# Kernel tuning notes

Measured on AMD Instinct MI355X. Metric: run time of the kernel, lower is better.

Reference implementation:

```python
import jax, jax.numpy as jnp
import numpy as np

EPS = 1e-6
N = 512
D = 8192


def solve_lap_np(cost):
    """Jonker-Volgenant shortest-augmenting-path LAP (same optimum as
    scipy.optimize.linear_sum_assignment). Returns col4row: col assigned to each row."""
    cost = np.asarray(cost, dtype=np.float64)
    n = cost.shape[0]
    u = np.zeros(n)
    v = np.zeros(n)
    path = np.full(n, -1, dtype=np.int64)
    col4row = np.full(n, -1, dtype=np.int64)
    row4col = np.full(n, -1, dtype=np.int64)
    for cur_row in range(n):
        shortest = np.full(n, np.inf)
        SR = np.zeros(n, dtype=bool)  # visited rows
        SC = np.zeros(n, dtype=bool)  # visited cols
        i = cur_row
        min_val = 0.0
        sink = -1
        while sink == -1:
            SR[i] = True
            idx = np.nonzero(~SC)[0]
            r = min_val + cost[i, idx] - u[i] - v[idx]
            upd = r < shortest[idx]
            shortest[idx[upd]] = r[upd]
            path[idx[upd]] = i
            j = idx[np.argmin(shortest[idx])]
            min_val = shortest[j]
            SC[j] = True
            if row4col[j] == -1:
                sink = j
            else:
                i = row4col[j]
        # dual updates
        u[cur_row] += min_val
        sr = np.nonzero(SR)[0]
        sr = sr[sr != cur_row]
        u[sr] += min_val - shortest[col4row[sr]]
        sc = np.nonzero(SC)[0]
        v[sc] -= min_val - shortest[sc]
        # augment along the alternating path
        j = sink
        while True:
            i = path[j]
            row4col[j] = i
            col4row[i], j = j, col4row[i]
            if i == cur_row:
                break
    return col4row


def lap_assign(cost):
    """Optimal assignment as a one-hot labelling matrix (rows -> cols)."""
    n = cost.shape[0]
    col = jax.pure_callback(
        lambda c: solve_lap_np(np.asarray(c)).astype(np.int32),
        jax.ShapeDtypeStruct((n,), jnp.int32),
        cost,
    )
    return jax.nn.one_hot(col, n, dtype=cost.dtype)


def l2_normalize(x):
    # torch F.normalize(p=2, dim=1): x / max(||x||, eps)
    norm = jnp.sqrt(jnp.sum(x * x, axis=1, keepdims=True))
    return x / jnp.maximum(norm, EPS)


def setup_inputs() -> dict:
    key = jax.random.key(0)
    k1, k2, k3 = jax.random.split(key, 3)
    return {
        "un1": jax.random.normal(k1, (N, D), dtype=jnp.float32),
        "un2": jax.random.normal(k2, (N, D), dtype=jnp.float32),
        "un3": jax.random.normal(k3, (N, D), dtype=jnp.float32),
    }


def reference(un1, un2, un3):
    n1 = l2_normalize(un1)
    n2 = l2_normalize(un2)
    n3 = l2_normalize(un3)
    # cosine-distance cost matrices, cycle 1->2->3->1
    c12 = 1.0 - n1 @ n2.T
    c23 = 1.0 - n2 @ n3.T
    c31 = 1.0 - n3 @ n1.T
    x12 = lap_assign(c12)
    x23 = lap_assign(c23)
    x31 = lap_assign(c31)
    return (x12, x23, x31)
```

## Files before the change

kernel.cpp:

```cpp
#include <hip/hip_runtime.h>
#include <math.h>

#define NN 512
#define DD 8192

__global__ __launch_bounds__(256) void norm_kernel(
    const float* __restrict__ a0, const float* __restrict__ a1,
    const float* __restrict__ a2, float* __restrict__ scales) {
  const float* mats[3] = {a0, a1, a2};
  const int m = blockIdx.y;
  const int row = blockIdx.x;
  const float* x = mats[m] + (size_t)row * DD;
  const int tid = threadIdx.x;
  float s = 0.f;
  for (int k = tid * 4; k < DD; k += 256 * 4) {
    const float4 v = *(const float4*)(x + k);
    s += v.x * v.x + v.y * v.y + v.z * v.z + v.w * v.w;
  }
#pragma unroll
  for (int off = 32; off > 0; off >>= 1) s += __shfl_down(s, off);
  __shared__ float ws[4];
  if ((tid & 63) == 0) ws[tid >> 6] = s;
  __syncthreads();
  if (tid == 0) {
    const float t = ws[0] + ws[1] + ws[2] + ws[3];
    scales[m * NN + row] = 1.0f / fmaxf(sqrtf(t), 1e-6f);
  }
}

__global__ __launch_bounds__(512) void cost_gemm_kernel(
    const float* __restrict__ a0, const float* __restrict__ a1,
    const float* __restrict__ a2, const float* __restrict__ scales,
    float* __restrict__ cost_all) {
  const float* mats[3] = {a0, a1, a2};
  const int p = blockIdx.z;
  const int pA = p, pB = (p + 1) % 3;
  const float* A = mats[pA];
  const float* B = mats[pB];
  float* C = cost_all + (size_t)p * NN * NN;

  __shared__ float lds_a[32 * 64];
  __shared__ float lds_b[32 * 64];

  const int tid = threadIdx.x;
  const int rowBase = blockIdx.y * 64;
  const int colBase = blockIdx.x * 64;

  const int sr = tid & 63;
  const int sk = (tid >> 6) * 4;

  const float* Arow = A + (size_t)(rowBase + sr) * DD + sk;
  const float* Brow = B + (size_t)(colBase + sr) * DD + sk;

  const int tx = tid & 31;
  const int ty = tid >> 5;

  float acc[4][2];
#pragma unroll
  for (int i = 0; i < 4; ++i) {
    acc[i][0] = 0.f;
    acc[i][1] = 0.f;
  }

  for (int kb = 0; kb < DD; kb += 32) {
    const float4 av = *(const float4*)(Arow + kb);
    const float4 bv = *(const float4*)(Brow + kb);
    lds_a[(sk + 0) * 64 + sr] = av.x;
    lds_a[(sk + 1) * 64 + sr] = av.y;
    lds_a[(sk + 2) * 64 + sr] = av.z;
    lds_a[(sk + 3) * 64 + sr] = av.w;
    lds_b[(sk + 0) * 64 + sr] = bv.x;
    lds_b[(sk + 1) * 64 + sr] = bv.y;
    lds_b[(sk + 2) * 64 + sr] = bv.z;
    lds_b[(sk + 3) * 64 + sr] = bv.w;
    __syncthreads();
#pragma unroll
    for (int k = 0; k < 32; ++k) {
      const float4 a4 = *(const float4*)(&lds_a[k * 64 + ty * 4]);
      const float2 b2 = *(const float2*)(&lds_b[k * 64 + tx * 2]);
      const float as0[4] = {a4.x, a4.y, a4.z, a4.w};
#pragma unroll
      for (int ii = 0; ii < 4; ++ii) {
        acc[ii][0] = fmaf(as0[ii], b2.x, acc[ii][0]);
        acc[ii][1] = fmaf(as0[ii], b2.y, acc[ii][1]);
      }
    }
    __syncthreads();
  }

#pragma unroll
  for (int ii = 0; ii < 4; ++ii) {
    const int gr = rowBase + ty * 4 + ii;
    const float sa = scales[pA * NN + gr];
#pragma unroll
    for (int jj = 0; jj < 2; ++jj) {
      const int gc = colBase + tx * 2 + jj;
      const float sb = scales[pB * NN + gc];
      C[gr * NN + gc] = 1.0f - acc[ii][jj] * sa * sb;
    }
  }
}


__device__ __forceinline__ int SW(int c) { return ((c & 7) << 6) | (c >> 3); }

__device__ __forceinline__ unsigned wave_min_u32(unsigned x) {
  int t;
  t = __builtin_amdgcn_update_dpp((int)x, (int)x, 0x111, 0xf, 0xf, false);
  x = ((unsigned)t < x) ? (unsigned)t : x;
  t = __builtin_amdgcn_update_dpp((int)x, (int)x, 0x112, 0xf, 0xf, false);
  x = ((unsigned)t < x) ? (unsigned)t : x;
  t = __builtin_amdgcn_update_dpp((int)x, (int)x, 0x114, 0xf, 0xf, false);
  x = ((unsigned)t < x) ? (unsigned)t : x;
  t = __builtin_amdgcn_update_dpp((int)x, (int)x, 0x118, 0xf, 0xf, false);
  x = ((unsigned)t < x) ? (unsigned)t : x;
  t = __builtin_amdgcn_update_dpp((int)x, (int)x, 0x142, 0xf, 0xf, false);
  x = ((unsigned)t < x) ? (unsigned)t : x;
  t = __builtin_amdgcn_update_dpp((int)x, (int)x, 0x143, 0xf, 0xf, false);
  x = ((unsigned)t < x) ? (unsigned)t : x;
  return (unsigned)__builtin_amdgcn_readlane((int)x, 63);
}

__device__ __forceinline__ double readlane_f64(double x, int lane) {
  const long long b = __double_as_longlong(x);
  const int lo = __builtin_amdgcn_readlane((int)(b & 0xffffffffLL), lane);
  const int hi = __builtin_amdgcn_readlane((int)(b >> 32), lane);
  return __longlong_as_double(((long long)hi << 32) | (unsigned long long)(unsigned)lo);
}

__device__ __forceinline__ unsigned long long f64key(double x) {
  const long long b = __double_as_longlong(x);
  return (b < 0) ? ~(unsigned long long)b
                 : ((unsigned long long)b | 0x8000000000000000ULL);
}

__global__ __launch_bounds__(64) void lap_kernel(
    const float* __restrict__ cost_all, float* __restrict__ out) {
  const int p = blockIdx.x;
  const float* cost = cost_all + (size_t)p * NN * NN;
  float* outp = out + (size_t)p * NN * NN;
  const int tid = threadIdx.x;

  __shared__ double sh_u[NN];
  __shared__ double sh_shortest[NN];
  __shared__ int sh_path[NN];
  __shared__ int sh_x[NN];
  __shared__ int sh_y[NN];

  const double INF = __builtin_inf();

#pragma unroll
  for (int q = 0; q < 8; ++q) {
    const int e = tid * 8 + q;
    sh_x[SW(e)] = -1;
    sh_y[SW(e)] = -1;
    sh_u[SW(e)] = 0.0;
  }
  double myV[8];
#pragma unroll
  for (int q = 0; q < 8; ++q) myV[q] = 0.0;
  __syncthreads();

  for (int cur_row = 0; cur_row < NN; ++cur_row) {
    double selv[8];
    double vAdj[8];
    double frz[8];
    int myPath[8];
    unsigned pl[8];
#pragma unroll
    for (int q = 0; q < 8; ++q) {
      selv[q] = INF;
      vAdj[q] = myV[q];
      frz[q] = 0.0;
      myPath[q] = 0;
    }
#pragma unroll
    for (int q = 0; q < 8; ++q)
      pl[q] = ((unsigned)q << 10) | (unsigned)(sh_y[SW(tid * 8 + q)] + 1);

    unsigned scMask = 0, srMask = 0;
    int i = cur_row;
    double minv = 0.0;
    int sink = -1;
    int pendQ = -1, pendLane = 0;

    while (true) {
      const float4 c0 = *(const float4*)(cost + (size_t)i * NN + tid * 8);
      const float4 c1 = *(const float4*)(cost + (size_t)i * NN + tid * 8 + 4);
      const double u_i = sh_u[SW(i)];
      if ((i >> 3) == tid) srMask |= 1u << (i & 7);
      if (pendQ >= 0) {
        const bool me = (tid == pendLane);
#define APPLY_SC(K)                                                     \
        if (pendQ == K) {                                               \
          if (me) {                                                     \
            selv[K] = INF; vAdj[K] = -INF; frz[K] = minv;               \
            scMask |= 1u << K;                                          \
          }                                                             \
        }
        APPLY_SC(0) APPLY_SC(1) APPLY_SC(2) APPLY_SC(3)
        APPLY_SC(4) APPLY_SC(5) APPLY_SC(6) APPLY_SC(7)
#undef APPLY_SC
      }
      const double mu = minv - u_i;
      double base[8];
#pragma unroll
      for (int q = 0; q < 8; ++q) base[q] = mu - vAdj[q];
      const float cf[8] = {c0.x, c0.y, c0.z, c0.w, c1.x, c1.y, c1.z, c1.w};
#pragma unroll
      for (int q = 0; q < 8; ++q) {
        const double r = (double)cf[q] + base[q];
        const bool cnd = r < selv[q];
        selv[q] = fmin(selv[q], r);
        myPath[q] = cnd ? i : myPath[q];
      }
      const bool t01 = selv[1] < selv[0];
      double v01 = t01 ? selv[1] : selv[0]; unsigned p01 = t01 ? pl[1] : pl[0];
      const bool t23 = selv[3] < selv[2];
      double v23 = t23 ? selv[3] : selv[2]; unsigned p23 = t23 ? pl[3] : pl[2];
      const bool t45 = selv[5] < selv[4];
      double v45 = t45 ? selv[5] : selv[4]; unsigned p45 = t45 ? pl[5] : pl[4];
      const bool t67 = selv[7] < selv[6];
      double v67 = t67 ? selv[7] : selv[6]; unsigned p67 = t67 ? pl[7] : pl[6];
      const bool ta = v23 < v01;
      const double vab = ta ? v23 : v01; const unsigned pab = ta ? p23 : p01;
      const bool tb = v67 < v45;
      const double vcd = tb ? v67 : v45; const unsigned pcd = tb ? p67 : p45;
      const bool tc = vcd < vab;
      const double lv = tc ? vcd : vab; const unsigned lp = tc ? pcd : pab;
      const unsigned long long kk = f64key(lv);
      const unsigned hi = (unsigned)(kk >> 32);
      const unsigned lo = (unsigned)kk;
      const unsigned minhi = wave_min_u32(hi);
      unsigned long long bal = __ballot(hi == minhi);
      int srcLane;
      if (__popcll(bal) == 1) {
        srcLane = __ffsll(bal) - 1;
      } else {
        const unsigned lo2 = (hi == minhi) ? lo : 0xFFFFFFFFu;
        const unsigned minlo = wave_min_u32(lo2);
        bal = __ballot((hi == minhi) && (lo == minlo));
        srcLane = __ffsll(bal) - 1;
      }
      const unsigned pw = (unsigned)__builtin_amdgcn_readlane((int)lp, srcLane);
      const int qb = (int)(pw >> 10);
      const int r4 = (int)(pw & 0x3FFu) - 1;
      minv = readlane_f64(lv, srcLane);
      if (r4 < 0) {
        sink = srcLane * 8 + qb;
        break;
      }
      i = r4;
      pendQ = qb;
      pendLane = srcLane;
    }

#pragma unroll
    for (int q = 0; q < 8; ++q) {
      sh_shortest[SW(tid * 8 + q)] = frz[q];
      sh_path[SW(tid * 8 + q)] = myPath[q];
    }
    __syncthreads();
#pragma unroll
    for (int q = 0; q < 8; ++q) {
      const int row = tid * 8 + q;
      if (row == cur_row) {
        sh_u[SW(row)] += minv;
      } else if (srMask & (1u << q)) {
        sh_u[SW(row)] += minv - sh_shortest[SW(sh_x[SW(row)])];
      }
      if (scMask & (1u << q)) myV[q] -= minv - frz[q];
    }
    __syncthreads();
    if (tid == 0) {
      int j = sink;
      while (true) {
        const int pi = sh_path[SW(j)];
        sh_y[SW(j)] = pi;
        const int tmp = sh_x[SW(pi)];
        sh_x[SW(pi)] = j;
        j = tmp;
        if (pi == cur_row) break;
      }
    }
    __syncthreads();
  }

#pragma unroll
  for (int q = 0; q < 8; ++q) {
    const int row = tid * 8 + q;
    outp[(size_t)row * NN + sh_x[SW(row)]] = 1.0f;
  }
}

extern "C" void kernel_launch(void* const* d_in, const int* in_sizes, int n_in,
                              void* d_out, int out_size, void* d_ws, size_t ws_size,
                              hipStream_t stream) {
  const float* un1 = (const float*)d_in[0];
  const float* un2 = (const float*)d_in[1];
  const float* un3 = (const float*)d_in[2];
  float* out = (float*)d_out;

  float* cost = (float*)d_ws;
  float* scales = cost + (size_t)3 * NN * NN;

  hipMemsetAsync(d_out, 0, (size_t)out_size * sizeof(float), stream);

  norm_kernel<<<dim3(NN, 3), 256, 0, stream>>>(un1, un2, un3, scales);
  cost_gemm_kernel<<<dim3(NN / 64, NN / 64, 3), 512, 0, stream>>>(un1, un2, un3, scales, cost);
  lap_kernel<<<3, 64, 0, stream>>>(cost, out);
}
```

Measured before the change: 5.753 ms.

## Use fp32 argmin keys with fp64 fallback and defer fp64 relaxation update

Picks the argmin column in each Dijkstra step of the LAP solver by comparing 32-bit float keys (one wave_min instead of a two-stage 64-bit min). It falls back to the exact fp64 reduction when several candidates lie within a few ULPs of each other. The fp64 update of shortest/path is deferred to the next iteration, so it overlaps with the next row's cost load and the reduction stays off its critical path. The risk is near-tie handling: if the ULP tolerance misses a case, the chosen column could differ from the fp64 optimum.

```diff
diff --git a/kernel.cpp b/kernel.cpp
--- a/kernel.cpp
+++ b/kernel.cpp
@@ -134,6 +134,36 @@
                  : ((unsigned long long)b | 0x8000000000000000ULL);
 }
 
+__device__ __forceinline__ unsigned f32key(float x) {
+  const int b = __float_as_int(x);
+  return (b < 0) ? ~(unsigned)b : ((unsigned)b | 0x80000000u);
+}
+
+#define TREE8(v, pq, oV, oP)                                                   \
+  do {                                                                         \
+    const bool t01 = (v)[1] < (v)[0];                                          \
+    const double a0 = t01 ? (v)[1] : (v)[0];                                   \
+    const unsigned b0 = t01 ? (pq)[1] : (pq)[0];                               \
+    const bool t23 = (v)[3] < (v)[2];                                          \
+    const double a1 = t23 ? (v)[3] : (v)[2];                                   \
+    const unsigned b1 = t23 ? (pq)[3] : (pq)[2];                               \
+    const bool t45 = (v)[5] < (v)[4];                                          \
+    const double a2 = t45 ? (v)[5] : (v)[4];                                   \
+    const unsigned b2 = t45 ? (pq)[5] : (pq)[4];                               \
+    const bool t67 = (v)[7] < (v)[6];                                          \
+    const double a3 = t67 ? (v)[7] : (v)[6];                                   \
+    const unsigned b3 = t67 ? (pq)[7] : (pq)[6];                               \
+    const bool ta = a1 < a0;                                                   \
+    const double c0_ = ta ? a1 : a0;                                           \
+    const unsigned d0_ = ta ? b1 : b0;                                         \
+    const bool tb = a3 < a2;                                                   \
+    const double c1_ = tb ? a3 : a2;                                           \
+    const unsigned d1_ = tb ? b3 : b2;                                         \
+    const bool tc = c1_ < c0_;                                                 \
+    (oV) = tc ? c1_ : c0_;                                                     \
+    (oP) = tc ? d1_ : d0_;                                                     \
+  } while (0)
+
 __global__ __launch_bounds__(64) void lap_kernel(
     const float* __restrict__ cost_all, float* __restrict__ out) {
   const int p = blockIdx.x;
@@ -148,6 +178,7 @@
   __shared__ int sh_y[NN];
 
   const double INF = __builtin_inf();
+  const float INFF = __builtin_inff();
 
 #pragma unroll
   for (int q = 0; q < 8; ++q) {
@@ -165,13 +196,21 @@
     double selv[8];
     double vAdj[8];
     double frz[8];
+    double base[8];
+    double baseP[8];
+    float cfP[8];
+    float base32[8];
+    float selv32[8];
     int myPath[8];
     unsigned pl[8];
 #pragma unroll
     for (int q = 0; q < 8; ++q) {
       selv[q] = INF;
+      selv32[q] = INFF;
       vAdj[q] = myV[q];
       frz[q] = 0.0;
+      baseP[q] = INF;
+      cfP[q] = 0.f;
       myPath[q] = 0;
     }
 #pragma unroll
@@ -182,6 +221,7 @@
     int i = cur_row;
     double minv = 0.0;
     int sink = -1;
+    int iPrev = 0;
     int pendQ = -1, pendLane = 0;
 
     while (true) {
@@ -189,7 +229,20 @@
       const float4 c1 = *(const float4*)(cost + (size_t)i * NN + tid * 8 + 4);
       const double u_i = sh_u[SW(i)];
       if ((i >> 3) == tid) srMask |= 1u << (i & 7);
+
+#pragma unroll
+      for (int q = 0; q < 8; ++q) {
+        const double rp = (double)cfP[q] + baseP[q];
+        const bool cnd = rp < selv[q];
+        myPath[q] = cnd ? iPrev : myPath[q];
+        selv[q] = fmin(selv[q], rp);
+      }
       if (pendQ >= 0) {
+        double sval = 0.0;
+#define EXTV(K) if (pendQ == K) sval = selv[K];
+        EXTV(0) EXTV(1) EXTV(2) EXTV(3) EXTV(4) EXTV(5) EXTV(6) EXTV(7)
+#undef EXTV
+        minv = readlane_f64(sval, pendLane);
         const bool me = (tid == pendLane);
 #define APPLY_SC(K)                                                     \
         if (pendQ == K) {                                               \
@@ -203,56 +256,101 @@
 #undef APPLY_SC
       }
       const double mu = minv - u_i;
-      double base[8];
-#pragma unroll
-      for (int q = 0; q < 8; ++q) base[q] = mu - vAdj[q];
+#pragma unroll
+      for (int q = 0; q < 8; ++q) {
+        base[q] = mu - vAdj[q];
+        base32[q] = (float)base[q];
+        selv32[q] = (float)selv[q];
+      }
+
       const float cf[8] = {c0.x, c0.y, c0.z, c0.w, c1.x, c1.y, c1.z, c1.w};
+      unsigned k[8];
 #pragma unroll
       for (int q = 0; q < 8; ++q) {
-        const double r = (double)cf[q] + base[q];
-        const bool cnd = r < selv[q];
-        selv[q] = fmin(selv[q], r);
-        myPath[q] = cnd ? i : myPath[q];
-      }
-      const bool t01 = selv[1] < selv[0];
-      double v01 = t01 ? selv[1] : selv[0]; unsigned p01 = t01 ? pl[1] : pl[0];
-      const bool t23 = selv[3] < selv[2];
-      double v23 = t23 ? selv[3] : selv[2]; unsigned p23 = t23 ? pl[3] : pl[2];
-      const bool t45 = selv[5] < selv[4];
-      double v45 = t45 ? selv[5] : selv[4]; unsigned p45 = t45 ? pl[5] : pl[4];
-      const bool t67 = selv[7] < selv[6];
-      double v67 = t67 ? selv[7] : selv[6]; unsigned p67 = t67 ? pl[7] : pl[6];
-      const bool ta = v23 < v01;
-      const double vab = ta ? v23 : v01; const unsigned pab = ta ? p23 : p01;
-      const bool tb = v67 < v45;
-      const double vcd = tb ? v67 : v45; const unsigned pcd = tb ? p67 : p45;
-      const bool tc = vcd < vab;
-      const double lv = tc ? vcd : vab; const unsigned lp = tc ? pcd : pab;
-      const unsigned long long kk = f64key(lv);
-      const unsigned hi = (unsigned)(kk >> 32);
-      const unsigned lo = (unsigned)kk;
-      const unsigned minhi = wave_min_u32(hi);
-      unsigned long long bal = __ballot(hi == minhi);
-      int srcLane;
-      if (__popcll(bal) == 1) {
-        srcLane = __ffsll(bal) - 1;
-      } else {
-        const unsigned lo2 = (hi == minhi) ? lo : 0xFFFFFFFFu;
-        const unsigned minlo = wave_min_u32(lo2);
-        bal = __ballot((hi == minhi) && (lo == minlo));
-        srcLane = __ffsll(bal) - 1;
-      }
-      const unsigned pw = (unsigned)__builtin_amdgcn_readlane((int)lp, srcLane);
-      const int qb = (int)(pw >> 10);
+        const float r32 = cf[q] + base32[q];
+        const float cand = fminf(selv32[q], r32);
+        k[q] = f32key(cand);
+      }
+      const bool s01 = k[1] < k[0];
+      const unsigned ka = s01 ? k[1] : k[0]; const unsigned pa = s01 ? pl[1] : pl[0];
+      const bool s23 = k[3] < k[2];
+      const unsigned kb2 = s23 ? k[3] : k[2]; const unsigned pb = s23 ? pl[3] : pl[2];
+      const bool s45 = k[5] < k[4];
+      const unsigned kc = s45 ? k[5] : k[4]; const unsigned pc = s45 ? pl[5] : pl[4];
+      const bool s67 = k[7] < k[6];
+      const unsigned kd = s67 ? k[7] : k[6]; const unsigned pd = s67 ? pl[7] : pl[6];
+      const bool sA = kb2 < ka;
+      const unsigned kab = sA ? kb2 : ka; const unsigned pab = sA ? pb : pa;
+      const bool sB = kd < kc;
+      const unsigned kcd = sB ? kd : kc; const unsigned pcd = sB ? pd : pc;
+      const bool sC = kcd < kab;
+      const unsigned bk = sC ? kcd : kab; const unsigned bp = sC ? pcd : pab;
+      int cnt = 0;
+#pragma unroll
+      for (int q = 0; q < 8; ++q) cnt += (k[q] <= bk + 4u) ? 1 : 0;
+      const unsigned gk = wave_min_u32(bk);
+      const unsigned long long near = __ballot(bk <= gk + 4u);
+      int srcLane = 0;
+      unsigned pw = 0;
+      bool slow = (__popcll(near) != 1);
+      if (!slow) {
+        srcLane = __ffsll(near) - 1;
+        const unsigned flagged = bp | ((cnt > 1) ? 0x80000000u : 0u);
+        pw = (unsigned)__builtin_amdgcn_readlane((int)flagged, srcLane);
+        slow = (pw >> 31) != 0;
+      }
+      if (slow) {
+        double m64[8];
+#pragma unroll
+        for (int q = 0; q < 8; ++q) {
+          const double r64 = (double)cf[q] + base[q];
+          m64[q] = fmin(selv[q], r64);
+        }
+        double lv;
+        unsigned lp;
+        TREE8(m64, pl, lv, lp);
+        const unsigned long long kk = f64key(lv);
+        const unsigned hi = (unsigned)(kk >> 32);
+        const unsigned lo = (unsigned)kk;
+        const unsigned minhi = wave_min_u32(hi);
+        unsigned long long bal = __ballot(hi == minhi);
+        if (__popcll(bal) == 1) {
+          srcLane = __ffsll(bal) - 1;
+        } else {
+          const unsigned lo2 = (hi == minhi) ? lo : 0xFFFFFFFFu;
+          const unsigned minlo = wave_min_u32(lo2);
+          bal = __ballot((hi == minhi) && (lo == minlo));
+          srcLane = __ffsll(bal) - 1;
+        }
+        pw = (unsigned)__builtin_amdgcn_readlane((int)lp, srcLane);
+      }
+      const int qb = (int)((pw >> 10) & 7u);
       const int r4 = (int)(pw & 0x3FFu) - 1;
-      minv = readlane_f64(lv, srcLane);
+#pragma unroll
+      for (int q = 0; q < 8; ++q) { cfP[q] = cf[q]; baseP[q] = base[q]; }
+      iPrev = i;
+      pendQ = qb;
+      pendLane = srcLane;
       if (r4 < 0) {
         sink = srcLane * 8 + qb;
         break;
       }
       i = r4;
-      pendQ = qb;
-      pendLane = srcLane;
+    }
+
+#pragma unroll
+    for (int q = 0; q < 8; ++q) {
+      const double rp = (double)cfP[q] + baseP[q];
+      const bool cnd = rp < selv[q];
+      myPath[q] = cnd ? iPrev : myPath[q];
+      selv[q] = fmin(selv[q], rp);
+    }
+    {
+      double sval = 0.0;
+#define EXTV(K) if (pendQ == K) sval = selv[K];
+      EXTV(0) EXTV(1) EXTV(2) EXTV(3) EXTV(4) EXTV(5) EXTV(6) EXTV(7)
+#undef EXTV
+      minv = readlane_f64(sval, pendLane);
     }
 
 #pragma unroll
```

Measured after the change: 7.539 ms. 31.0% more time.
